# Kernel tuning notes

Hardware: AMD Instinct MI355X
Metric: run time of the kernel (lower is better)

The kernel has to match this reference:

```python
import jax, jax.numpy as jnp
import numpy as np

HIDDEN = 2048
N_HEADS = 16
HEAD_DIM = HIDDEN // N_HEADS  # 128
BATCH = 2
SEQ = 2048


def setup_inputs() -> dict:
    key = jax.random.key(0)
    ks = jax.random.split(key, 9)
    std = HIDDEN ** -0.5
    inp = {
        "hidden_states": jax.random.normal(ks[0], (BATCH, SEQ, HIDDEN), dtype=jnp.float32),
        "q_w": jax.random.normal(ks[1], (HIDDEN, HIDDEN), dtype=jnp.float32) * std,
        "k_w": jax.random.normal(ks[2], (HIDDEN, HIDDEN), dtype=jnp.float32) * std,
        "v_w": jax.random.normal(ks[3], (HIDDEN, HIDDEN), dtype=jnp.float32) * std,
        "o_w": jax.random.normal(ks[4], (HIDDEN, HIDDEN), dtype=jnp.float32) * std,
        "q_b": jnp.zeros((HIDDEN,), dtype=jnp.float32),
        "k_b": jnp.zeros((HIDDEN,), dtype=jnp.float32),
        "v_b": jnp.zeros((HIDDEN,), dtype=jnp.float32),
        "o_b": jnp.zeros((HIDDEN,), dtype=jnp.float32),
    }
    return inp


def reference(hidden_states, q_w, k_w, v_w, o_w, q_b, k_b, v_b, o_b):
    b, s, _ = hidden_states.shape
    # Projections (nn.Linear applies x @ W^T + b); split heads -> [b, h, s, d]
    def proj(w, bias):
        y = hidden_states @ w.T + bias
        return y.reshape(b, s, N_HEADS, HEAD_DIM).transpose(0, 2, 1, 3)

    q = proj(q_w, q_b)
    k = proj(k_w, k_b)
    v = proj(v_w, v_b)

    scale = 1.0 / jnp.sqrt(jnp.float32(HEAD_DIM))
    scores = jnp.einsum("bhqd,bhkd->bhqk", q, k) * scale  # [b, h, s, s]

    # causal mask: mask positions where k > q (triu, diagonal=1)
    qi = jnp.arange(s)[:, None]
    ki = jnp.arange(s)[None, :]
    scores = jnp.where(ki > qi, -jnp.inf, scores)

    attn = jax.nn.softmax(scores.astype(jnp.float32), axis=-1).astype(q.dtype)
    out = jnp.einsum("bhqk,bhkd->bhqd", attn, v)
    out = out.transpose(0, 2, 1, 3).reshape(b, s, HIDDEN)
    return out @ o_w.T + o_b
```

## Files before the change

kernel.cpp:

```cpp
#include <hip/hip_runtime.h>

#define S_HID 2048
#define S_SEQ 2048
#define S_B   2
#define S_NH  16
#define S_HD  128
#define S_M   (S_B * S_SEQ)
#define S_BH  (S_B * S_NH)

typedef __bf16 bf16_t;
typedef __bf16 bf16x8 __attribute__((ext_vector_type(8)));
typedef __bf16 bf16x4 __attribute__((ext_vector_type(4)));
typedef float  floatx4 __attribute__((ext_vector_type(4)));
typedef float  floatx16 __attribute__((ext_vector_type(16)));

typedef __attribute__((address_space(1))) unsigned int as1_uint;
typedef __attribute__((address_space(3))) unsigned int as3_uint;

__device__ __forceinline__ void gload_lds16(const void* g, void* l) {
    __builtin_amdgcn_global_load_lds((as1_uint*)g, (as3_uint*)l, 16, 0, 0);
}

__global__ void cvt_all(const float* __restrict__ x,
                        const float* __restrict__ qw, const float* __restrict__ kw,
                        const float* __restrict__ vw, const float* __restrict__ ow,
                        bf16_t* __restrict__ Xb, bf16_t* __restrict__ Wqkv) {
    const int XV = (S_M * S_HID) >> 2;
    const int WV = (S_HID * S_HID) >> 2;
    const int total = XV + 4 * WV;
    int stride = gridDim.x * blockDim.x;
    for (int i = blockIdx.x * blockDim.x + threadIdx.x; i < total; i += stride) {
        const float* src;
        bf16x4* dst;
        int local;
        if (i < XV) {
            src = x; local = i; dst = (bf16x4*)Xb;
        } else {
            int j = i - XV;
            int r = j >> 20;
            local = j & (WV - 1);
            src = r == 0 ? qw : r == 1 ? kw : r == 2 ? vw : ow;
            dst = (bf16x4*)Wqkv + (size_t)r * WV;
        }
        float4 v = ((const float4*)src)[local];
        bf16x4 o;
        o.x = (bf16_t)v.x; o.y = (bf16_t)v.y; o.z = (bf16_t)v.z; o.w = (bf16_t)v.w;
        dst[local] = o;
    }
}

__global__ __launch_bounds__(256, 3)
void gemm_qkv(const bf16_t* __restrict__ A, const bf16_t* __restrict__ W,
              const float* __restrict__ qbias, const float* __restrict__ kbias,
              const float* __restrict__ vbias,
              bf16_t* __restrict__ Qo, bf16_t* __restrict__ Ko, bf16_t* __restrict__ Vto,
              float qscale) {
    __shared__ __align__(16) bf16_t ldsA[128 * 64];
    __shared__ __align__(16) bf16_t ldsB[128 * 64];
    const int tid = threadIdx.x;
    const int wid = tid >> 6, lane = tid & 63;
    const int m0 = blockIdx.y * 128, n0 = blockIdx.x * 128;
    const int wm = (wid & 1) * 64, wn = (wid >> 1) * 64;
    const int lm = lane & 15, quad = lane >> 4;
    const int srow = lane >> 3;
    const int scol = lane & 7;

    floatx4 acc[4][4];
    #pragma unroll
    for (int i = 0; i < 4; ++i)
        #pragma unroll
        for (int j = 0; j < 4; ++j)
            acc[i][j] = (floatx4){0.f, 0.f, 0.f, 0.f};

    for (int kt = 0; kt < S_HID; kt += 64) {
        #pragma unroll
        for (int i = 0; i < 4; ++i) {
            int slot = i * 4 + wid;
            int row = slot * 8 + srow;
            int cg = scol ^ (row & 7);
            gload_lds16(A + (size_t)(m0 + row) * S_HID + kt + cg * 8, &ldsA[slot * 512]);
            gload_lds16(W + (size_t)(n0 + row) * S_HID + kt + cg * 8, &ldsB[slot * 512]);
        }
        __syncthreads();
        #pragma unroll
        for (int k2 = 0; k2 < 2; ++k2) {
            bf16x8 af[4], bfr[4];
            #pragma unroll
            for (int i = 0; i < 4; ++i) {
                int row = wm + i * 16 + lm;
                int cc = (k2 * 4 + quad) ^ (row & 7);
                af[i] = *(const bf16x8*)&ldsA[row * 64 + cc * 8];
            }
            #pragma unroll
            for (int j = 0; j < 4; ++j) {
                int row = wn + j * 16 + lm;
                int cc = (k2 * 4 + quad) ^ (row & 7);
                bfr[j] = *(const bf16x8*)&ldsB[row * 64 + cc * 8];
            }
            #pragma unroll
            for (int i = 0; i < 4; ++i)
                #pragma unroll
                for (int j = 0; j < 4; ++j)
                    acc[i][j] = __builtin_amdgcn_mfma_f32_16x16x32_bf16(af[i], bfr[j], acc[i][j], 0, 0, 0);
        }
        __syncthreads();
    }

    const int region = n0 >> 11;
    if (region < 2) {
        bf16_t* Ob = region ? Ko : Qo;
        const float* bias = region ? kbias : qbias;
        float scale = region ? 1.0f : qscale;
        #pragma unroll
        for (int i = 0; i < 4; ++i) {
            #pragma unroll
            for (int j = 0; j < 4; ++j) {
                int n = n0 + wn + j * 16 + lm;
                float bv = bias[n & 2047];
                int nl = n & 2047;
                int h = nl >> 7, d = nl & 127;
                #pragma unroll
                for (int r = 0; r < 4; ++r) {
                    int m = m0 + wm + i * 16 + quad * 4 + r;
                    int b = m >> 11, s = m & 2047;
                    Ob[(((size_t)(b * S_NH + h)) * S_SEQ + s) * S_HD + d] =
                        (bf16_t)((acc[i][j][r] + bv) * scale);
                }
            }
        }
    } else {
        #pragma unroll
        for (int i = 0; i < 4; ++i) {
            #pragma unroll
            for (int j = 0; j < 4; ++j) {
                int n = n0 + wn + j * 16 + lm;
                int nl = n & 2047;
                float bv = vbias[nl];
                int h = nl >> 7, d = nl & 127;
                int m = m0 + wm + i * 16 + quad * 4;
                int b = m >> 11, s = m & 2047;
                bf16x4 ov;
                #pragma unroll
                for (int r = 0; r < 4; ++r) ov[r] = (bf16_t)(acc[i][j][r] + bv);
                *(bf16x4*)&Vto[(((size_t)(b * S_NH + h)) * S_HD + d) * S_SEQ + s] = ov;
            }
        }
    }
}

__global__ __launch_bounds__(256, 3)
void gemm_out(const bf16_t* __restrict__ A, const bf16_t* __restrict__ W,
              const float* __restrict__ bias, float* __restrict__ out) {
    __shared__ __align__(16) bf16_t ldsA[128 * 64];
    __shared__ __align__(16) bf16_t ldsB[128 * 64];
    const int tid = threadIdx.x;
    const int wid = tid >> 6, lane = tid & 63;
    const int m0 = blockIdx.y * 128, n0 = blockIdx.x * 128;
    const int wm = (wid & 1) * 64, wn = (wid >> 1) * 64;
    const int lm = lane & 15, quad = lane >> 4;
    const int srow = lane >> 3;
    const int scol = lane & 7;

    floatx4 acc[4][4];
    #pragma unroll
    for (int i = 0; i < 4; ++i)
        #pragma unroll
        for (int j = 0; j < 4; ++j)
            acc[i][j] = (floatx4){0.f, 0.f, 0.f, 0.f};

    for (int kt = 0; kt < S_HID; kt += 64) {
        #pragma unroll
        for (int i = 0; i < 4; ++i) {
            int slot = i * 4 + wid;
            int row = slot * 8 + srow;
            int cg = scol ^ (row & 7);
            gload_lds16(A + (size_t)(m0 + row) * S_HID + kt + cg * 8, &ldsA[slot * 512]);
            gload_lds16(W + (size_t)(n0 + row) * S_HID + kt + cg * 8, &ldsB[slot * 512]);
        }
        __syncthreads();
        #pragma unroll
        for (int k2 = 0; k2 < 2; ++k2) {
            bf16x8 af[4], bfr[4];
            #pragma unroll
            for (int i = 0; i < 4; ++i) {
                int row = wm + i * 16 + lm;
                int cc = (k2 * 4 + quad) ^ (row & 7);
                af[i] = *(const bf16x8*)&ldsA[row * 64 + cc * 8];
            }
            #pragma unroll
            for (int j = 0; j < 4; ++j) {
                int row = wn + j * 16 + lm;
                int cc = (k2 * 4 + quad) ^ (row & 7);
                bfr[j] = *(const bf16x8*)&ldsB[row * 64 + cc * 8];
            }
            #pragma unroll
            for (int i = 0; i < 4; ++i)
                #pragma unroll
                for (int j = 0; j < 4; ++j)
                    acc[i][j] = __builtin_amdgcn_mfma_f32_16x16x32_bf16(af[i], bfr[j], acc[i][j], 0, 0, 0);
        }
        __syncthreads();
    }

    #pragma unroll
    for (int i = 0; i < 4; ++i) {
        #pragma unroll
        for (int j = 0; j < 4; ++j) {
            int n = n0 + wn + j * 16 + lm;
            float bv = bias[n];
            #pragma unroll
            for (int r = 0; r < 4; ++r) {
                int m = m0 + wm + i * 16 + quad * 4 + r;
                out[(size_t)m * S_HID + n] = acc[i][j][r] + bv;
            }
        }
    }
}

__device__ __forceinline__ bf16x8 make_pfrag(bf16x4 lo, bf16x4 hi, int h) {
    int2 li = __builtin_bit_cast(int2, lo);
    int2 hh = __builtin_bit_cast(int2, hi);
    int2 xl, xh;
    xl.x = __shfl_xor(li.x, 32); xl.y = __shfl_xor(li.y, 32);
    xh.x = __shfl_xor(hh.x, 32); xh.y = __shfl_xor(hh.y, 32);
    int2 flo, fhi;
    flo.x = h ? xh.x : li.x;  flo.y = h ? xh.y : li.y;
    fhi.x = h ? hh.x : xl.x;  fhi.y = h ? hh.y : xl.y;
    bf16x4 a = __builtin_bit_cast(bf16x4, flo);
    bf16x4 b = __builtin_bit_cast(bf16x4, fhi);
    return __builtin_shufflevector(a, b, 0, 1, 2, 3, 4, 5, 6, 7);
}

__global__ __launch_bounds__(256, 2)
void attn(const bf16_t* __restrict__ Q, const bf16_t* __restrict__ K,
          const bf16_t* __restrict__ Vt, bf16_t* __restrict__ O) {
    __shared__ __align__(16) bf16_t ldsK[2][64 * 128];
    __shared__ __align__(16) bf16_t ldsV[2][128 * 64];
    const int tid = threadIdx.x, wid = tid >> 6, lane = tid & 63;
    const int lm = lane & 15, quad = lane >> 4;
    const int srow = lane >> 3, scol = lane & 7;
    const int c31 = lane & 31, h = lane >> 5, r7 = lane & 7;
    const int bx = blockIdx.x;
    const int bh = bx & 31, idx = bx >> 5;
    const int qt = idx < 8 ? idx : 23 - idx;
    const int q0 = qt * 128;
    const int b = bh >> 4, hd = bh & 15;

    const bf16_t* Kbase = K + (size_t)bh * S_SEQ * S_HD;
    const bf16_t* Vbase = Vt + (size_t)bh * S_HD * S_SEQ;

    const int qcol = q0 + wid * 32 + c31;
    const int nkt = qt * 2 + 2;

    bf16x8 qf[8];
    {
        const bf16_t* qp = Q + ((size_t)bh * S_SEQ + qcol) * S_HD + h * 8;
        #pragma unroll
        for (int ks = 0; ks < 8; ++ks) qf[ks] = *(const bf16x8*)(qp + ks * 16);
    }

    floatx16 oa[4];
    #pragma unroll
    for (int jd = 0; jd < 4; ++jd)
        #pragma unroll
        for (int e = 0; e < 16; ++e) oa[jd][e] = 0.f;
    float m_st = -1e30f, l_st = 0.f;

    #pragma unroll
    for (int i = 0; i < 4; ++i) {
        int slot = i * 4 + wid;
        int krow = slot * 4 + quad;
        int kcg = lm ^ (krow & 7);
        gload_lds16(Kbase + (size_t)krow * S_HD + kcg * 8, &ldsK[0][slot * 512]);
        int vrow = slot * 8 + srow;
        int vcg = scol ^ (vrow & 7);
        gload_lds16(Vbase + (size_t)vrow * S_SEQ + vcg * 8, &ldsV[0][slot * 512]);
    }

    int pp = 0;
    for (int kti = 0; kti < nkt; ++kti) {
        const int kt = kti * 64;
        __syncthreads();

        if (kti + 1 < nkt) {
            const int ktn = kt + 64;
            #pragma unroll
            for (int i = 0; i < 4; ++i) {
                int slot = i * 4 + wid;
                int krow = slot * 4 + quad;
                int kcg = lm ^ (krow & 7);
                gload_lds16(Kbase + (size_t)(ktn + krow) * S_HD + kcg * 8, &ldsK[pp ^ 1][slot * 512]);
                int vrow = slot * 8 + srow;
                int vcg = scol ^ (vrow & 7);
                gload_lds16(Vbase + (size_t)vrow * S_SEQ + ktn + vcg * 8, &ldsV[pp ^ 1][slot * 512]);
            }
        }

        floatx16 sa[2];
        #pragma unroll
        for (int jr = 0; jr < 2; ++jr)
            #pragma unroll
            for (int e = 0; e < 16; ++e) sa[jr][e] = 0.f;
        #pragma unroll
        for (int ks = 0; ks < 8; ++ks) {
            #pragma unroll
            for (int jr = 0; jr < 2; ++jr) {
                int row = jr * 32 + c31;
                bf16x8 kf = *(const bf16x8*)&ldsK[pp][row * 128 + (((ks * 2 + h) ^ r7)) * 8];
                sa[jr] = __builtin_amdgcn_mfma_f32_32x32x16_bf16(kf, qf[ks], sa[jr], 0, 0, 0);
            }
        }

        if (kti >= nkt - 2) {
            #pragma unroll
            for (int jr = 0; jr < 2; ++jr)
                #pragma unroll
                for (int rr = 0; rr < 16; ++rr) {
                    int key = kt + jr * 32 + (rr & 3) + 8 * (rr >> 2) + 4 * h;
                    if (key > qcol) sa[jr][rr] = -1e30f;
                }
        }

        float mx = -1e30f;
        #pragma unroll
        for (int jr = 0; jr < 2; ++jr)
            #pragma unroll
            for (int rr = 0; rr < 16; ++rr) mx = fmaxf(mx, sa[jr][rr]);
        mx = fmaxf(mx, __shfl_xor(mx, 32));
        float mn = fmaxf(m_st, mx);
        float al = __builtin_amdgcn_exp2f(m_st - mn);
        m_st = mn;

        float rs = 0.f;
        bf16x8 pf[4];
        #pragma unroll
        for (int jr = 0; jr < 2; ++jr) {
            bf16x4 pk[4];
            #pragma unroll
            for (int g = 0; g < 4; ++g)
                #pragma unroll
                for (int e = 0; e < 4; ++e) {
                    float p = __builtin_amdgcn_exp2f(sa[jr][g * 4 + e] - mn);
                    rs += p;
                    pk[g][e] = (bf16_t)p;
                }
            pf[jr * 2]     = make_pfrag(pk[0], pk[1], h);
            pf[jr * 2 + 1] = make_pfrag(pk[2], pk[3], h);
        }
        rs += __shfl_xor(rs, 32);
        l_st = l_st * al + rs;
        #pragma unroll
        for (int jd = 0; jd < 4; ++jd)
            #pragma unroll
            for (int e = 0; e < 16; ++e) oa[jd][e] *= al;

        #pragma unroll
        for (int kb = 0; kb < 4; ++kb) {
            #pragma unroll
            for (int jd = 0; jd < 4; ++jd) {
                int row = jd * 32 + c31;
                bf16x8 vf = *(const bf16x8*)&ldsV[pp][row * 64 + (((kb * 2 + h) ^ r7)) * 8];
                oa[jd] = __builtin_amdgcn_mfma_f32_32x32x16_bf16(vf, pf[kb], oa[jd], 0, 0, 0);
            }
        }
        pp ^= 1;
    }

    float inv = 1.0f / l_st;
    bf16_t* op = O + ((size_t)b * S_SEQ + qcol) * S_HID + hd * S_HD;
    #pragma unroll
    for (int jd = 0; jd < 4; ++jd)
        #pragma unroll
        for (int g = 0; g < 4; ++g) {
            bf16x4 ov;
            #pragma unroll
            for (int e = 0; e < 4; ++e) ov[e] = (bf16_t)(oa[jd][g * 4 + e] * inv);
            *(bf16x4*)&op[jd * 32 + g * 8 + 4 * h] = ov;
        }
}

extern "C" void kernel_launch(void* const* d_in, const int* in_sizes, int n_in,
                              void* d_out, int out_size, void* d_ws, size_t ws_size,
                              hipStream_t stream) {
    const float* hs = (const float*)d_in[0];
    const float* qw = (const float*)d_in[1];
    const float* kw = (const float*)d_in[2];
    const float* vw = (const float*)d_in[3];
    const float* ow = (const float*)d_in[4];
    const float* qbias = (const float*)d_in[5];
    const float* kbias = (const float*)d_in[6];
    const float* vbias = (const float*)d_in[7];
    const float* obias = (const float*)d_in[8];

    char* ws = (char*)d_ws;
    bf16_t* Xb   = (bf16_t*)(ws + 0);
    bf16_t* Wqkv = (bf16_t*)(ws + 16777216);
    bf16_t* Wob  = (bf16_t*)(ws + 41943040);
    bf16_t* Qb   = (bf16_t*)(ws + 50331648);
    bf16_t* Kb   = (bf16_t*)(ws + 67108864);
    bf16_t* Vtb  = (bf16_t*)(ws + 83886080);
    bf16_t* Ob   = Xb;

    cvt_all<<<2048, 256, 0, stream>>>(hs, qw, kw, vw, ow, Xb, Wqkv);

    const float qscale = 0.08838834764831845f * 1.4426950408889634f;
    gemm_qkv<<<dim3(48, 32), 256, 0, stream>>>(Xb, Wqkv, qbias, kbias, vbias,
                                               Qb, Kb, Vtb, qscale);

    attn<<<512, 256, 0, stream>>>(Qb, Kb, Vtb, Ob);

    gemm_out<<<dim3(16, 32), 256, 0, stream>>>(Ob, Wob, obias, (float*)d_out);
}
```

Measured before the change: 367.0 us.

## Rewrite QKV GEMM with 256x256 tiles, 8 waves, double-buffered LDS pipeline

The QKV projection GEMM moves from 128x128 tiles with 4 waves and a single LDS buffer to 256x256 tiles with 8 waves. It adds a double-buffered LDS pipeline that issues the next k-tile's global-to-LDS loads while the current tile's MFMAs run, using explicit vmcnt waits, split barriers and s_setprio around the MFMA bursts. The larger tile cuts global traffic per FLOP and the overlap hides load latency. In exchange it uses 128KB of LDS and more accumulator registers per block, and the grid shrinks to 384 blocks, which may leave the 256 CUs unevenly loaded.

```diff
diff --git a/kernel.cpp b/kernel.cpp
--- a/kernel.cpp
+++ b/kernel.cpp
@@ -49,62 +49,132 @@
     }
 }
 
-__global__ __launch_bounds__(256, 3)
+__global__ __launch_bounds__(512, 2)
 void gemm_qkv(const bf16_t* __restrict__ A, const bf16_t* __restrict__ W,
               const float* __restrict__ qbias, const float* __restrict__ kbias,
               const float* __restrict__ vbias,
               bf16_t* __restrict__ Qo, bf16_t* __restrict__ Ko, bf16_t* __restrict__ Vto,
               float qscale) {
-    __shared__ __align__(16) bf16_t ldsA[128 * 64];
-    __shared__ __align__(16) bf16_t ldsB[128 * 64];
+    __shared__ __align__(16) bf16_t lds[2][2][2][256 * 32];
     const int tid = threadIdx.x;
     const int wid = tid >> 6, lane = tid & 63;
-    const int m0 = blockIdx.y * 128, n0 = blockIdx.x * 128;
-    const int wm = (wid & 1) * 64, wn = (wid >> 1) * 64;
+    const int wr = wid >> 2, wc = wid & 3;
     const int lm = lane & 15, quad = lane >> 4;
-    const int srow = lane >> 3;
-    const int scol = lane & 7;
-
-    floatx4 acc[4][4];
-    #pragma unroll
-    for (int i = 0; i < 4; ++i)
+    const int m0 = blockIdx.y * 256, n0 = blockIdx.x * 256;
+
+    const int s_r = lane >> 2;
+    const int s_g = (lane & 3) ^ ((lane >> 3) & 3);
+    const bf16_t* srcA = A + (size_t)(m0 + wid * 32 + s_r) * S_HID + s_g * 8;
+    const bf16_t* srcB = W + (size_t)(n0 + wid * 32 + s_r) * S_HID + s_g * 8;
+    const int slot0 = (wid * 2) * 512;
+    const int slot1 = (wid * 2 + 1) * 512;
+
+    const int flm = (lm >> 1) & 3;
+    const int roA = (wr * 128 + lm) * 32 + (quad ^ flm) * 8;
+    const int roB = (wc * 64 + lm) * 32 + (quad ^ flm) * 8;
+
+    floatx4 acc[8][4];
+    #pragma unroll
+    for (int i = 0; i < 8; ++i)
         #pragma unroll
         for (int j = 0; j < 4; ++j)
             acc[i][j] = (floatx4){0.f, 0.f, 0.f, 0.f};
 
-    for (int kt = 0; kt < S_HID; kt += 64) {
-        #pragma unroll
-        for (int i = 0; i < 4; ++i) {
-            int slot = i * 4 + wid;
-            int row = slot * 8 + srow;
-            int cg = scol ^ (row & 7);
-            gload_lds16(A + (size_t)(m0 + row) * S_HID + kt + cg * 8, &ldsA[slot * 512]);
-            gload_lds16(W + (size_t)(n0 + row) * S_HID + kt + cg * 8, &ldsB[slot * 512]);
-        }
-        __syncthreads();
-        #pragma unroll
-        for (int k2 = 0; k2 < 2; ++k2) {
-            bf16x8 af[4], bfr[4];
-            #pragma unroll
-            for (int i = 0; i < 4; ++i) {
-                int row = wm + i * 16 + lm;
-                int cc = (k2 * 4 + quad) ^ (row & 7);
-                af[i] = *(const bf16x8*)&ldsA[row * 64 + cc * 8];
-            }
-            #pragma unroll
-            for (int j = 0; j < 4; ++j) {
-                int row = wn + j * 16 + lm;
-                int cc = (k2 * 4 + quad) ^ (row & 7);
-                bfr[j] = *(const bf16x8*)&ldsB[row * 64 + cc * 8];
-            }
-            #pragma unroll
-            for (int i = 0; i < 4; ++i)
-                #pragma unroll
-                for (int j = 0; j < 4; ++j)
-                    acc[i][j] = __builtin_amdgcn_mfma_f32_16x16x32_bf16(af[i], bfr[j], acc[i][j], 0, 0, 0);
-        }
-        __syncthreads();
-    }
+#define STAGE(SRC, BUF, MAT, K2, KT) do {                                             \
+        gload_lds16((SRC) + (KT) + (K2) * 32,         &lds[BUF][MAT][K2][slot0]);     \
+        gload_lds16((SRC) + 32768 + (KT) + (K2) * 32, &lds[BUF][MAT][K2][slot1]);     \
+    } while (0)
+
+#define MFMA16(IOFF) do {                                                             \
+        __builtin_amdgcn_s_setprio(1);                                                \
+        _Pragma("unroll")                                                             \
+        for (int i_ = 0; i_ < 4; ++i_)                                                \
+            _Pragma("unroll")                                                         \
+            for (int j_ = 0; j_ < 4; ++j_)                                            \
+                acc[(IOFF) + i_][j_] = __builtin_amdgcn_mfma_f32_16x16x32_bf16(       \
+                    af[i_], bfr[j_], acc[(IOFF) + i_][j_], 0, 0, 0);                  \
+        __builtin_amdgcn_s_setprio(0);                                                \
+    } while (0)
+
+    STAGE(srcA, 0, 0, 0, 0);
+    STAGE(srcB, 0, 1, 0, 0);
+    STAGE(srcA, 0, 0, 1, 0);
+    STAGE(srcB, 0, 1, 1, 0);
+    asm volatile("s_waitcnt vmcnt(4)" ::: "memory");
+    __builtin_amdgcn_s_barrier();
+
+    bf16x8 af[4], bfr[4];
+    for (int t = 0; t < 31; ++t) {
+        const int b = t & 1, nb = b ^ 1;
+        const int ktn = (t + 1) * 64;
+
+        STAGE(srcA, nb, 0, 0, ktn);
+        #pragma unroll
+        for (int i = 0; i < 4; ++i) af[i] = *(const bf16x8*)&lds[b][0][0][roA + i * 512];
+        #pragma unroll
+        for (int j = 0; j < 4; ++j) bfr[j] = *(const bf16x8*)&lds[b][1][0][roB + j * 512];
+        __builtin_amdgcn_s_barrier();
+        MFMA16(0);
+        __builtin_amdgcn_s_barrier();
+
+        STAGE(srcB, nb, 1, 0, ktn);
+        #pragma unroll
+        for (int i = 0; i < 4; ++i) af[i] = *(const bf16x8*)&lds[b][0][0][roA + (i + 4) * 512];
+        __builtin_amdgcn_s_barrier();
+        MFMA16(4);
+        asm volatile("s_waitcnt vmcnt(4)" ::: "memory");
+        __builtin_amdgcn_s_barrier();
+
+        STAGE(srcA, nb, 0, 1, ktn);
+        #pragma unroll
+        for (int i = 0; i < 4; ++i) af[i] = *(const bf16x8*)&lds[b][0][1][roA + i * 512];
+        #pragma unroll
+        for (int j = 0; j < 4; ++j) bfr[j] = *(const bf16x8*)&lds[b][1][1][roB + j * 512];
+        __builtin_amdgcn_s_barrier();
+        MFMA16(0);
+        __builtin_amdgcn_s_barrier();
+
+        STAGE(srcB, nb, 1, 1, ktn);
+        #pragma unroll
+        for (int i = 0; i < 4; ++i) af[i] = *(const bf16x8*)&lds[b][0][1][roA + (i + 4) * 512];
+        __builtin_amdgcn_s_barrier();
+        MFMA16(4);
+        asm volatile("s_waitcnt vmcnt(4)" ::: "memory");
+        __builtin_amdgcn_s_barrier();
+    }
+
+    {
+        const int b = 1;
+        #pragma unroll
+        for (int i = 0; i < 4; ++i) af[i] = *(const bf16x8*)&lds[b][0][0][roA + i * 512];
+        #pragma unroll
+        for (int j = 0; j < 4; ++j) bfr[j] = *(const bf16x8*)&lds[b][1][0][roB + j * 512];
+        __builtin_amdgcn_s_barrier();
+        MFMA16(0);
+        __builtin_amdgcn_s_barrier();
+
+        #pragma unroll
+        for (int i = 0; i < 4; ++i) af[i] = *(const bf16x8*)&lds[b][0][0][roA + (i + 4) * 512];
+        __builtin_amdgcn_s_barrier();
+        MFMA16(4);
+        asm volatile("s_waitcnt vmcnt(0)" ::: "memory");
+        __builtin_amdgcn_s_barrier();
+
+        #pragma unroll
+        for (int i = 0; i < 4; ++i) af[i] = *(const bf16x8*)&lds[b][0][1][roA + i * 512];
+        #pragma unroll
+        for (int j = 0; j < 4; ++j) bfr[j] = *(const bf16x8*)&lds[b][1][1][roB + j * 512];
+        __builtin_amdgcn_s_barrier();
+        MFMA16(0);
+        __builtin_amdgcn_s_barrier();
+
+        #pragma unroll
+        for (int i = 0; i < 4; ++i) af[i] = *(const bf16x8*)&lds[b][0][1][roA + (i + 4) * 512];
+        __builtin_amdgcn_s_barrier();
+        MFMA16(4);
+    }
+#undef STAGE
+#undef MFMA16
 
     const int region = n0 >> 11;
     if (region < 2) {
@@ -112,37 +182,37 @@
         const float* bias = region ? kbias : qbias;
         float scale = region ? 1.0f : qscale;
         #pragma unroll
-        for (int i = 0; i < 4; ++i) {
+        for (int i = 0; i < 8; ++i) {
             #pragma unroll
             for (int j = 0; j < 4; ++j) {
-                int n = n0 + wn + j * 16 + lm;
-                float bv = bias[n & 2047];
+                int n = n0 + wc * 64 + j * 16 + lm;
                 int nl = n & 2047;
+                float bv = bias[nl];
                 int h = nl >> 7, d = nl & 127;
                 #pragma unroll
                 for (int r = 0; r < 4; ++r) {
-                    int m = m0 + wm + i * 16 + quad * 4 + r;
-                    int b = m >> 11, s = m & 2047;
-                    Ob[(((size_t)(b * S_NH + h)) * S_SEQ + s) * S_HD + d] =
+                    int m = m0 + wr * 128 + i * 16 + quad * 4 + r;
+                    int bb = m >> 11, s = m & 2047;
+                    Ob[(((size_t)(bb * S_NH + h)) * S_SEQ + s) * S_HD + d] =
                         (bf16_t)((acc[i][j][r] + bv) * scale);
                 }
             }
         }
     } else {
         #pragma unroll
-        for (int i = 0; i < 4; ++i) {
+        for (int i = 0; i < 8; ++i) {
             #pragma unroll
             for (int j = 0; j < 4; ++j) {
-                int n = n0 + wn + j * 16 + lm;
+                int n = n0 + wc * 64 + j * 16 + lm;
                 int nl = n & 2047;
                 float bv = vbias[nl];
                 int h = nl >> 7, d = nl & 127;
-                int m = m0 + wm + i * 16 + quad * 4;
-                int b = m >> 11, s = m & 2047;
+                int m = m0 + wr * 128 + i * 16 + quad * 4;
+                int bb = m >> 11, s = m & 2047;
                 bf16x4 ov;
                 #pragma unroll
                 for (int r = 0; r < 4; ++r) ov[r] = (bf16_t)(acc[i][j][r] + bv);
-                *(bf16x4*)&Vto[(((size_t)(b * S_NH + h)) * S_HD + d) * S_SEQ + s] = ov;
+                *(bf16x4*)&Vto[(((size_t)(bb * S_NH + h)) * S_HD + d) * S_SEQ + s] = ov;
             }
         }
     }
@@ -404,7 +474,7 @@
     cvt_all<<<2048, 256, 0, stream>>>(hs, qw, kw, vw, ow, Xb, Wqkv);
 
     const float qscale = 0.08838834764831845f * 1.4426950408889634f;
-    gemm_qkv<<<dim3(48, 32), 256, 0, stream>>>(Xb, Wqkv, qbias, kbias, vbias,
+    gemm_qkv<<<dim3(24, 16), 512, 0, stream>>>(Xb, Wqkv, qbias, kbias, vbias,
                                                Qb, Kb, Vtb, qscale);
 
     attn<<<512, 256, 0, stream>>>(Qb, Kb, Vtb, Ob);
```

Result: no change. 366.3 us (-0.2%).
